# Optimization experiments

Hardware: AMD Instinct MI355X
Metric: run time of the kernel (lower is better)

The kernel has to match this reference:

```python
import jax, jax.numpy as jnp
import numpy as np

B, T, D = 2, 2048, 1024
H = 16
HD = D // H  # head_dim = 64 (kv_rank == embed_dim)
INT4_MIN, INT4_MAX = -8.0, 7.0


def _int4_quant_dequant(x):
    # per-token amax over last dim (head_dim), as in INT4Quantizer with 4-D input
    amax = jnp.max(jnp.abs(x), axis=-1, keepdims=True)
    amax = jnp.maximum(amax, 1e-5)
    scale = amax / 7.0
    q = jnp.clip(jnp.round(x / scale), INT4_MIN, INT4_MAX)  # stored as int8 in cache
    return q * scale


def setup_inputs() -> dict:
    key = jax.random.key(0)
    ks = jax.random.split(key, 11)
    s = 1.0 / np.sqrt(D)
    return {
        "query": jax.random.normal(ks[0], (B, T, D), jnp.float32),
        "key": jax.random.normal(ks[1], (B, T, D), jnp.float32),
        "value": jax.random.normal(ks[2], (B, T, D), jnp.float32),
        "Wq": jax.random.normal(ks[3], (D, D), jnp.float32) * s,
        "bq": jnp.zeros((D,), jnp.float32),
        "Wk": jax.random.normal(ks[4], (D, D), jnp.float32) * s,
        "bk": jnp.zeros((D,), jnp.float32),
        "Wv": jax.random.normal(ks[5], (D, D), jnp.float32) * s,
        "bv": jnp.zeros((D,), jnp.float32),
        "Wo": jax.random.normal(ks[6], (D, D), jnp.float32) * s,
        "bo": jnp.zeros((D,), jnp.float32),
    }


def reference(query, key, value, Wq, bq, Wk, bk, Wv, bv, Wo, bo):
    # projections (nn.Linear: x @ W.T + b)
    q = query @ Wq.T + bq
    k = key @ Wk.T + bk
    v = value @ Wv.T + bv
    # (B, T, D) -> (B, H, T, HD)
    q = q.reshape(B, T, H, HD).transpose(0, 2, 1, 3)
    k = k.reshape(B, T, H, HD).transpose(0, 2, 1, 3)
    v = v.reshape(B, T, H, HD).transpose(0, 2, 1, 3)
    # INT4 quantized KV cache update (use_cache=True): quantize -> scatter into
    # fresh cache -> dequantize the just-written block == quant/dequant of k, v
    k = _int4_quant_dequant(k)
    v = _int4_quant_dequant(v)
    # attention
    scale = HD ** (-0.5)
    attn = jnp.einsum("bhqd,bhkd->bhqk", q, k) * scale
    attn = jax.nn.softmax(attn.astype(jnp.float32), axis=-1).astype(query.dtype)
    out = jnp.einsum("bhqk,bhkd->bhqd", attn, v)
    out = out.transpose(0, 2, 1, 3).reshape(B, T, D)
    out = out @ Wo.T + bo
    return out
```

## Files before the change

### kernel.cpp

```cpp
#include <hip/hip_runtime.h>

typedef unsigned short u16;
typedef unsigned int u32;
typedef float f32x4 __attribute__((ext_vector_type(4)));
typedef float f32x16 __attribute__((ext_vector_type(16)));
typedef short s16x8 __attribute__((ext_vector_type(8)));
typedef u16 u16x8 __attribute__((ext_vector_type(8)));
typedef u16 u16x4 __attribute__((ext_vector_type(4)));
typedef u32 u32x4 __attribute__((ext_vector_type(4)));
typedef _Float16 h16x8 __attribute__((ext_vector_type(8)));
typedef _Float16 h16x2 __attribute__((ext_vector_type(2)));

#define B_ 2
#define T_ 2048
#define H_ 16
#define D_ 1024
#define HD_ 64
#define NTOK (B_*T_)

#define QSCALE 0.18033688011112042f

__device__ __forceinline__ u16 f2b(float f){
  u32 u = __float_as_uint(f);
  return (u16)((u + 0x7fffu + ((u>>16)&1u)) >> 16);
}
__device__ __forceinline__ float b2f(u16 h){ return __uint_as_float(((u32)h)<<16); }

__device__ __forceinline__ void gload_lds16(const u16* g, u16* s){
  __builtin_amdgcn_global_load_lds((const __attribute__((address_space(1))) void*)g,
                                   (__attribute__((address_space(3))) void*)s, 16, 0, 0);
}

template<int ROWS, int WAVES>
__device__ __forceinline__ void stage_tile(const u16* __restrict__ g, size_t ldg,
                                           u16* s, int tid){
  const int w = tid>>6, l = tid&63;
  const int rw = ROWS/WAVES;
  #pragma unroll
  for (int i=0;i<ROWS/(WAVES*8);i++){
    int r0 = w*rw + i*8;
    int r  = r0 + (l>>3);
    int u  = (l&7) ^ (r&7);
    gload_lds16(g + (size_t)r*ldg + (size_t)u*8, s + r0*64);
  }
}

__device__ __forceinline__ u16x8 rfragT(const u16* s, int r, int ks, int hi){
  int phys = (ks*2 + hi) ^ (r&7);
  return *(const u16x8*)(s + r*64 + phys*8);
}

__device__ __forceinline__ void stage_tile32(const u16* __restrict__ g, size_t ldg,
                                             u16* s, int tid){
  const int w = tid>>6, l = tid&63;
  int r0 = w*16;
  int r  = r0 + (l>>2);
  int v  = (l&3) ^ ((r>>1)&3);
  gload_lds16(g + (size_t)r*ldg + (size_t)v*8, s + r0*32);
}
__device__ __forceinline__ u16x8 read_frag32(const u16* s, int r, int l){
  int phys = (l>>4) ^ ((r>>1)&3);
  return *(const u16x8*)(s + r*32 + phys*8);
}

__device__ __forceinline__ f32x4 mfma16_bf16(u16x8 a, u16x8 b, f32x4 c){
  return __builtin_amdgcn_mfma_f32_16x16x32_bf16(
      __builtin_bit_cast(s16x8,a), __builtin_bit_cast(s16x8,b), c, 0,0,0);
}
__device__ __forceinline__ f32x16 mfma32_f16(u16x8 a, u16x8 b, f32x16 c){
  return __builtin_amdgcn_mfma_f32_32x32x16_f16(
      __builtin_bit_cast(h16x8,a), __builtin_bit_cast(h16x8,b), c, 0,0,0);
}

__device__ __forceinline__ float ex2(float x){
#if __has_builtin(__builtin_amdgcn_exp2f)
  return __builtin_amdgcn_exp2f(x);
#else
  return exp2f(x);
#endif
}
__device__ __forceinline__ u32 pk2(float a, float b){
  u16 x = __builtin_bit_cast(u16, (_Float16)a);
  u16 y = __builtin_bit_cast(u16, (_Float16)b);
  return (u32)x | ((u32)y<<16);
}
__device__ __forceinline__ u32 pkrtz(float a, float b){
#if __has_builtin(__builtin_amdgcn_cvt_pkrtz)
  auto r = __builtin_amdgcn_cvt_pkrtz(a, b);
  return __builtin_bit_cast(u32, r);
#else
  return pk2(a, b);
#endif
}

__device__ __forceinline__ void split_bf4(const float* in, u16* hi, u16* lo, int i){
  f32x4 v = ((const f32x4*)in)[i];
  u16x4 h, lw;
  #pragma unroll
  for (int j=0;j<4;j++){
    u16 hb = f2b(v[j]);
    h[j] = hb;
    lw[j] = f2b(v[j] - b2f(hb));
  }
  ((u16x4*)hi)[i] = h;
  ((u16x4*)lo)[i] = lw;
}
__device__ __forceinline__ void split_h4(const float* in, u16* out, int i){
  f32x4 v = ((const f32x4*)in)[i];
  u16x4 o;
  #pragma unroll
  for (int j=0;j<4;j++){
    _Float16 t = (_Float16)v[j];
    o[j] = __builtin_bit_cast(u16, t);
  }
  ((u16x4*)out)[i] = o;
}

__global__ void split_all_kernel(const float* __restrict__ q, const float* __restrict__ k,
                                 const float* __restrict__ v,
                                 const float* __restrict__ wq, const float* __restrict__ wk,
                                 const float* __restrict__ wv, const float* __restrict__ wo,
                                 u16* __restrict__ qh, u16* __restrict__ khi, u16* __restrict__ klo,
                                 u16* __restrict__ vhi, u16* __restrict__ vlo,
                                 u16* __restrict__ wqh, u16* __restrict__ wkh, u16* __restrict__ wkl,
                                 u16* __restrict__ wvh, u16* __restrict__ wvl, u16* __restrict__ woh){
  int i = blockIdx.x*256 + threadIdx.x;
  int which = blockIdx.y;
  if (which < 3){
    if (which==0)      split_h4 (q, qh, i);
    else if (which==1) split_bf4(k, khi, klo, i);
    else               split_bf4(v, vhi, vlo, i);
  } else {
    if (i >= D_*D_/4) return;
    if (which==3)      split_h4 (wq, wqh, i);
    else if (which==4) split_bf4(wk, wkh, wkl, i);
    else if (which==5) split_bf4(wv, wvh, wvl, i);
    else               split_h4 (wo, woh, i);
  }
}

template<int F16OUT>
__global__ __launch_bounds__(256)
void gemm1(const u16* __restrict__ Ah, const u16* __restrict__ Wh,
           const float* __restrict__ bias, void* __restrict__ Cout, float oscale)
{
  __shared__ u16 sA[2][128*64];
  __shared__ u16 sW[2][128*64];
  const int tid = threadIdx.x, l = tid&63, c = l&31, hi = l>>5, w = tid>>6;
  const int wm = w>>1, wn = w&1;
  const int bm = blockIdx.x, bn = blockIdx.y;
  const u16* A0 = Ah + (size_t)bm*128*D_;
  const u16* W0 = Wh + (size_t)bn*128*D_;
  f32x16 acc[2][2] = {};

  stage_tile<128,4>(A0, D_, sA[0], tid);
  stage_tile<128,4>(W0, D_, sW[0], tid);
  __syncthreads();
  for (int t=0; t<D_/64; ++t){
    const int cur = t&1;
    if (t+1 < D_/64){
      stage_tile<128,4>(A0 + (t+1)*64, D_, sA[cur^1], tid);
      stage_tile<128,4>(W0 + (t+1)*64, D_, sW[cur^1], tid);
    }
    #pragma unroll
    for (int kc=0;kc<4;kc++){
      u16x8 af[2], wf[2];
      af[0] = rfragT(sA[cur], wm*64 +      c, kc, hi);
      af[1] = rfragT(sA[cur], wm*64 + 32 + c, kc, hi);
      wf[0] = rfragT(sW[cur], wn*64 +      c, kc, hi);
      wf[1] = rfragT(sW[cur], wn*64 + 32 + c, kc, hi);
      #pragma unroll
      for (int mb=0;mb<2;mb++)
        #pragma unroll
        for (int nb=0;nb<2;nb++)
          acc[mb][nb] = mfma32_f16(af[mb], wf[nb], acc[mb][nb]);
    }
    __syncthreads();
  }

  #pragma unroll
  for (int nb=0;nb<2;nb++){
    int col = bn*128 + wn*64 + nb*32 + c;
    float bv = bias[col];
    #pragma unroll
    for (int mb=0;mb<2;mb++){
      #pragma unroll
      for (int r=0;r<16;r++){
        int row = bm*128 + wm*64 + mb*32 + (r&3) + 8*(r>>2) + 4*hi;
        float v = (acc[mb][nb][r] + bv) * oscale;
        if constexpr (F16OUT){
          ((_Float16*)Cout)[(size_t)row*D_ + col] = (_Float16)v;
        } else {
          ((float*)Cout)[(size_t)row*D_ + col] = v;
        }
      }
    }
  }
}

__global__ __launch_bounds__(512)
void gemm3_quant_kv(const u16* __restrict__ kAh, const u16* __restrict__ kAl,
                    const u16* __restrict__ kWh, const u16* __restrict__ kWl,
                    const float* __restrict__ kbias, u16* __restrict__ kOut,
                    const u16* __restrict__ vAh, const u16* __restrict__ vAl,
                    const u16* __restrict__ vWh, const u16* __restrict__ vWl,
                    const float* __restrict__ vbias, u16* __restrict__ vOut)
{
  extern __shared__ u16 sm[];
  const int tid = threadIdx.x, l = tid&63, w = tid>>6, l15 = l&15, g = l>>4;
  const int wm = w>>1, wn = w&1;
  const int bm = blockIdx.x, bn = blockIdx.y;
  const bool isV = blockIdx.z != 0;
  const u16* Ah = isV ? vAh : kAh;
  const u16* Al = isV ? vAl : kAl;
  const u16* Wh = isV ? vWh : kWh;
  const u16* Wl = isV ? vWl : kWl;
  const float* bias = isV ? vbias : kbias;
  u16* Out = isV ? vOut : kOut;

  const u16* A0 = Ah + (size_t)bm*128*D_;
  const u16* A1 = Al + (size_t)bm*128*D_;
  const u16* W0 = Wh + (size_t)bn*128*D_;
  const u16* W1 = Wl + (size_t)bn*128*D_;
  constexpr int TS = 128*32;
  f32x4 acc[2][4] = {};

  auto stage = [&](int buf, int t){
    u16* base = sm + buf*4*TS;
    stage_tile32(A0 + t*32, D_, base       , tid);
    stage_tile32(A1 + t*32, D_, base +   TS, tid);
    stage_tile32(W0 + t*32, D_, base + 2*TS, tid);
    stage_tile32(W1 + t*32, D_, base + 3*TS, tid);
  };
  stage(0,0);
  __syncthreads();
  for (int t=0; t<D_/32; ++t){
    const int cur = t&1;
    if (t+1 < D_/32) stage(cur^1, t+1);
    const u16* base = sm + cur*4*TS;
    u16x8 ahh[2], ahl[2], whh[4], whl[4];
    #pragma unroll
    for (int fm=0;fm<2;fm++){
      ahh[fm] = read_frag32(base     , wm*32+fm*16+l15, l);
      ahl[fm] = read_frag32(base+  TS, wm*32+fm*16+l15, l);
    }
    #pragma unroll
    for (int fn=0;fn<4;fn++){
      whh[fn] = read_frag32(base+2*TS, wn*64+fn*16+l15, l);
      whl[fn] = read_frag32(base+3*TS, wn*64+fn*16+l15, l);
    }
    #pragma unroll
    for (int fm=0;fm<2;fm++)
      #pragma unroll
      for (int fn=0;fn<4;fn++){
        acc[fm][fn] = mfma16_bf16(ahh[fm], whh[fn], acc[fm][fn]);
        acc[fm][fn] = mfma16_bf16(ahh[fm], whl[fn], acc[fm][fn]);
        acc[fm][fn] = mfma16_bf16(ahl[fm], whh[fn], acc[fm][fn]);
      }
    __syncthreads();
  }

  #pragma unroll
  for (int fn=0;fn<4;fn++){
    float bv = bias[bn*128 + wn*64 + fn*16 + l15];
    #pragma unroll
    for (int fm=0;fm<2;fm++)
      #pragma unroll
      for (int j=0;j<4;j++) acc[fm][fn][j] += bv;
  }

  u16 (*sdq)[136] = (u16(*)[136])sm;
  #pragma unroll
  for (int fm=0;fm<2;fm++)
    #pragma unroll
    for (int j=0;j<4;j++){
      float a = 0.f;
      #pragma unroll
      for (int fn=0;fn<4;fn++) a = fmaxf(a, fabsf(acc[fm][fn][j]));
      a = fmaxf(a, __shfl_xor(a,1)); a = fmaxf(a, __shfl_xor(a,2));
      a = fmaxf(a, __shfl_xor(a,4)); a = fmaxf(a, __shfl_xor(a,8));
      a = fmaxf(a, 1e-5f);
      float scale = a / 7.0f;
      int g2 = ((g&1)<<1) | (g>>1);
      int rowK = wm*32 + fm*16 + g*4  + j;
      int rowV = wm*32 + fm*16 + g2*4 + j;
      #pragma unroll
      for (int fn=0;fn<4;fn++){
        float q = rintf(acc[fm][fn][j] / scale);
        q = fminf(fmaxf(q, -8.f), 7.f);
        _Float16 dq = (_Float16)(q * scale);
        int col = wn*64 + fn*16 + l15;
        if (!isV) sdq[rowK][col] = __builtin_bit_cast(u16, dq);
        else      sdq[col][rowV] = __builtin_bit_cast(u16, dq);
      }
    }
  __syncthreads();

  if (!isV){
    int r = tid>>2, seg = tid&3;
    u16* dst = Out + (size_t)(bm*128 + r)*D_ + bn*128 + seg*32;
    #pragma unroll
    for (int i=0;i<4;i++)
      *(u16x8*)(dst + i*8) = *(const u16x8*)&sdq[r][seg*32 + i*8];
  } else {
    int cc = tid>>2, seg = tid&3;
    int hh = 2*bn + (cc>>6), dd = cc&63, b = bm>>4;
    u16* dst = Out + ((size_t)((b*H_+hh)*HD_ + dd))*T_ + (bm&15)*128 + seg*32;
    #pragma unroll
    for (int i=0;i<4;i++)
      *(u16x8*)(dst + i*8) = *(const u16x8*)&sdq[cc][seg*32 + i*8];
  }
}

__global__ __launch_bounds__(256, 4)
void attn_kernel(const _Float16* __restrict__ Qp, const u16* __restrict__ Kdq,
                 const u16* __restrict__ Vt, u16* __restrict__ po,
                 float* __restrict__ pl)
{
  __shared__ u16 sK[2][64*64];
  __shared__ u16 sV[2][64*64];
  const int tid = threadIdx.x, l = tid&63, c = l&31, hi = l>>5, w = tid>>6;
  const int dsp = blockIdx.x;
  const int xcd = dsp & 7, slot = dsp >> 3;
  const int bh = xcd*4 + (slot>>5);
  const int rem = slot & 31;
  const int qb = rem >> 1, sp = rem & 1;
  const int b = bh>>4, h = bh&15;

  u16x8 qf[4];
  {
    const u16* qrow = (const u16*)Qp + (size_t)(b*T_ + qb*128 + w*32 + c)*D_ + h*HD_;
    #pragma unroll
    for (int ks=0;ks<4;ks++)
      qf[ks] = *(const u16x8*)(qrow + ks*16 + hi*8);
  }

  f32x16 o0 = {}, o1 = {};
  float lsp = 0.f;

  const u16* Kb = Kdq + (size_t)(b*T_ + sp*1024)*D_ + h*HD_;
  const u16* Vb = Vt  + (size_t)(bh*HD_)*T_ + sp*1024;

  stage_tile<64,4>(Kb, D_, sK[0], tid);
  stage_tile<64,4>(Vb, T_, sV[0], tid);
  __syncthreads();

  for (int kt=0; kt<16; kt++){
    const int cur = kt&1;
    if (kt+1 < 16){
      stage_tile<64,4>(Kb + (size_t)((kt+1)*64)*D_, D_, sK[cur^1], tid);
      stage_tile<64,4>(Vb + (kt+1)*64,              T_, sV[cur^1], tid);
    }
    const u16* sKc = sK[cur];
    const u16* sVc = sV[cur];

    u16x8 vf0[4], vf1[4];
    #pragma unroll
    for (int ch=0; ch<4; ch++){
      vf0[ch] = rfragT(sVc,      c, ch, hi);
      vf1[ch] = rfragT(sVc, 32 + c, ch, hi);
    }

    #pragma unroll
    for (int kb=0;kb<2;kb++){
      f32x16 s = {};
      #pragma unroll
      for (int ks=0;ks<4;ks++){
        u16x8 kf = rfragT(sKc, kb*32 + c, ks, hi);
        s = mfma32_f16(kf, qf[ks], s);
      }
      float p[16];
      #pragma unroll
      for (int r=0;r<16;r++) p[r] = ex2(s[r]);
      {
        float t0 = (p[0]+p[1]) + (p[2]+p[3]);
        float t1 = (p[4]+p[5]) + (p[6]+p[7]);
        float t2 = (p[8]+p[9]) + (p[10]+p[11]);
        float t3 = (p[12]+p[13]) + (p[14]+p[15]);
        lsp += (t0+t1) + (t2+t3);
      }
      u32x4 pw0 = { pkrtz(p[0],p[1]),  pkrtz(p[2],p[3]),
                    pkrtz(p[4],p[5]),  pkrtz(p[6],p[7]) };
      u32x4 pw1 = { pkrtz(p[8],p[9]),  pkrtz(p[10],p[11]),
                    pkrtz(p[12],p[13]),pkrtz(p[14],p[15]) };
      u16x8 pa0 = __builtin_bit_cast(u16x8, pw0);
      u16x8 pa1 = __builtin_bit_cast(u16x8, pw1);
      o0 = mfma32_f16(pa0, vf0[kb*2+0], o0);
      o0 = mfma32_f16(pa1, vf0[kb*2+1], o0);
      o1 = mfma32_f16(pa0, vf1[kb*2+0], o1);
      o1 = mfma32_f16(pa1, vf1[kb*2+1], o1);
    }
    __syncthreads();
  }

  float lt = lsp + __shfl_xor(lsp, 32);
  if (hi == 0) pl[(size_t)(sp*32 + bh)*T_ + qb*128 + w*32 + c] = lt;

  u16* pob = po + ((size_t)(sp*32 + bh)*T_ + qb*128 + w*32)*HD_;
  #pragma unroll
  for (int r=0;r<16;r++){
    int crow = (r&3) + 8*(r>>2) + 4*hi;
    pob[crow*HD_ + c]      = __builtin_bit_cast(u16, (_Float16)o0[r]);
    pob[crow*HD_ + 32 + c] = __builtin_bit_cast(u16, (_Float16)o1[r]);
  }
}

__global__ __launch_bounds__(256)
void combine_kernel(const u16* __restrict__ po, const float* __restrict__ pl,
                    u16* __restrict__ Ao)
{
  const int dsp = blockIdx.x;
  const int xcd = dsp & 7, slot = dsp >> 3;
  const int bh = xcd*4 + (slot>>6);
  const int inner = slot & 63;
  int item = inner*256 + threadIdx.x;
  int d8 = item & 7, t = item >> 3;
  size_t r0 = ((size_t)bh*T_ + t);
  size_t r1 = r0 + (size_t)32*T_;
  h16x8 a = *(const h16x8*)(po + r0*HD_ + d8*8);
  h16x8 bb = *(const h16x8*)(po + r1*HD_ + d8*8);
  float lt = pl[r0] + pl[r1];
  float rl = 1.0f / lt;
  u16x8 o;
  #pragma unroll
  for (int j=0;j<8;j++)
    o[j] = __builtin_bit_cast(u16, (_Float16)(((float)a[j] + (float)bb[j])*rl));
  int b = bh>>4, h = bh&15;
  *(u16x8*)(Ao + ((size_t)(b*T_ + t))*D_ + h*HD_ + d8*8) = o;
}

extern "C" void kernel_launch(void* const* d_in, const int* in_sizes, int n_in,
                              void* d_out, int out_size, void* d_ws, size_t ws_size,
                              hipStream_t stream)
{
  (void)in_sizes; (void)n_in; (void)out_size; (void)ws_size;
  const float* query = (const float*)d_in[0];
  const float* key   = (const float*)d_in[1];
  const float* value = (const float*)d_in[2];
  const float* Wq = (const float*)d_in[3];
  const float* bq = (const float*)d_in[4];
  const float* Wk = (const float*)d_in[5];
  const float* bk = (const float*)d_in[6];
  const float* Wv = (const float*)d_in[7];
  const float* bv = (const float*)d_in[8];
  const float* Wo = (const float*)d_in[9];
  const float* bo = (const float*)d_in[10];
  float* out = (float*)d_out;

  char* p = (char*)d_ws;
  auto take = [&](size_t n){ char* r = p; p += (n + 255) & ~(size_t)255; return r; };
  const size_t big = (size_t)NTOK*D_*2;
  const size_t wsz = (size_t)D_*D_*2;

  u16* q_h  = (u16*)take(big);
  u16* khi  = (u16*)take(big);  u16* klo = (u16*)take(big);
  u16* vhi  = (u16*)take(big);  u16* vlo = (u16*)take(big);
  u16* wq_h = (u16*)take(wsz);
  u16* wkh  = (u16*)take(wsz);  u16* wkl = (u16*)take(wsz);
  u16* wvh  = (u16*)take(wsz);  u16* wvl = (u16*)take(wsz);
  u16* wo_h = (u16*)take(wsz);
  u16*  Qp  = (u16*)take(big);
  u16*  Kdq = (u16*)take(big);
  u16*  Vtp = (u16*)take(big);
  u16*  Ao  = (u16*)take(big);

  u16*   po = khi;
  float* pl = (float*)wq_h;

  split_all_kernel<<<dim3(NTOK*D_/4/256, 7), 256, 0, stream>>>(
      query, key, value, Wq, Wk, Wv, Wo,
      q_h, khi, klo, vhi, vlo,
      wq_h, wkh, wkl, wvh, wvl, wo_h);

  gemm1<1><<<dim3(32,8), 256, 0, stream>>>(q_h, wq_h, bq, Qp, QSCALE);

  gemm3_quant_kv<<<dim3(32,8,2), 512, 64*1024, stream>>>(
      khi, klo, wkh, wkl, bk, Kdq,
      vhi, vlo, wvh, wvl, bv, Vtp);

  attn_kernel<<<1024, 256, 0, stream>>>((const _Float16*)Qp, Kdq, Vtp, po, pl);
  combine_kernel<<<2048, 256, 0, stream>>>(po, pl, Ao);

  gemm1<0><<<dim3(32,8), 256, 0, stream>>>(Ao, wo_h, bo, out, 1.0f);
}
```

Baseline: 174.4 us.

## Fuse K/V fp32 to bf16 hi/lo split into the KV projection GEMM

The K and V activations are no longer pre-split into bf16 hi/lo buffers by the split kernel. The KV GEMM now stages the raw fp32 tiles into shared memory and does the hi/lo decomposition in registers while reading fragments. This removes a full read and two writes of the K/V activation tensors plus their re-read, at the cost of extra ALU work in the GEMM inner loop. The hi part is now formed by truncation rather than rounding, and the shared-memory layout changes to a swizzled fp32 A tile. The attention partial buffers get their own workspace because they can no longer alias the removed split buffers.

After: 173.9 us. About the same (-0.3%).

```diff
diff --git a/kernel.cpp b/kernel.cpp
--- a/kernel.cpp
+++ b/kernel.cpp
@@ -116,27 +116,20 @@
   ((u16x4*)out)[i] = o;
 }
 
-__global__ void split_all_kernel(const float* __restrict__ q, const float* __restrict__ k,
-                                 const float* __restrict__ v,
+__global__ void split_all_kernel(const float* __restrict__ q,
                                  const float* __restrict__ wq, const float* __restrict__ wk,
                                  const float* __restrict__ wv, const float* __restrict__ wo,
-                                 u16* __restrict__ qh, u16* __restrict__ khi, u16* __restrict__ klo,
-                                 u16* __restrict__ vhi, u16* __restrict__ vlo,
+                                 u16* __restrict__ qh,
                                  u16* __restrict__ wqh, u16* __restrict__ wkh, u16* __restrict__ wkl,
                                  u16* __restrict__ wvh, u16* __restrict__ wvl, u16* __restrict__ woh){
   int i = blockIdx.x*256 + threadIdx.x;
   int which = blockIdx.y;
-  if (which < 3){
-    if (which==0)      split_h4 (q, qh, i);
-    else if (which==1) split_bf4(k, khi, klo, i);
-    else               split_bf4(v, vhi, vlo, i);
-  } else {
-    if (i >= D_*D_/4) return;
-    if (which==3)      split_h4 (wq, wqh, i);
-    else if (which==4) split_bf4(wk, wkh, wkl, i);
-    else if (which==5) split_bf4(wv, wvh, wvl, i);
-    else               split_h4 (wo, woh, i);
-  }
+  if (which==0){ split_h4(q, qh, i); return; }
+  if (i >= D_*D_/4) return;
+  if (which==1)      split_h4 (wq, wqh, i);
+  else if (which==2) split_bf4(wk, wkh, wkl, i);
+  else if (which==3) split_bf4(wv, wvh, wvl, i);
+  else               split_h4 (wo, woh, i);
 }
 
 template<int F16OUT>
@@ -199,55 +192,67 @@
 }
 
 __global__ __launch_bounds__(512)
-void gemm3_quant_kv(const u16* __restrict__ kAh, const u16* __restrict__ kAl,
-                    const u16* __restrict__ kWh, const u16* __restrict__ kWl,
-                    const float* __restrict__ kbias, u16* __restrict__ kOut,
-                    const u16* __restrict__ vAh, const u16* __restrict__ vAl,
-                    const u16* __restrict__ vWh, const u16* __restrict__ vWl,
-                    const float* __restrict__ vbias, u16* __restrict__ vOut)
+void gemm3_quant_kv(const float* __restrict__ kA, const u16* __restrict__ kWh,
+                    const u16* __restrict__ kWl, const float* __restrict__ kbias,
+                    u16* __restrict__ kOut,
+                    const float* __restrict__ vA, const u16* __restrict__ vWh,
+                    const u16* __restrict__ vWl, const float* __restrict__ vbias,
+                    u16* __restrict__ vOut)
 {
   extern __shared__ u16 sm[];
   const int tid = threadIdx.x, l = tid&63, w = tid>>6, l15 = l&15, g = l>>4;
   const int wm = w>>1, wn = w&1;
   const int bm = blockIdx.x, bn = blockIdx.y;
   const bool isV = blockIdx.z != 0;
-  const u16* Ah = isV ? vAh : kAh;
-  const u16* Al = isV ? vAl : kAl;
+  const float* Af = isV ? vA : kA;
   const u16* Wh = isV ? vWh : kWh;
   const u16* Wl = isV ? vWl : kWl;
   const float* bias = isV ? vbias : kbias;
   u16* Out = isV ? vOut : kOut;
 
-  const u16* A0 = Ah + (size_t)bm*128*D_;
-  const u16* A1 = Al + (size_t)bm*128*D_;
+  const u16* A0u = (const u16*)(Af + (size_t)bm*128*D_);
   const u16* W0 = Wh + (size_t)bn*128*D_;
   const u16* W1 = Wl + (size_t)bn*128*D_;
-  constexpr int TS = 128*32;
+  constexpr int BUF = 16384;
   f32x4 acc[2][4] = {};
 
   auto stage = [&](int buf, int t){
-    u16* base = sm + buf*4*TS;
-    stage_tile32(A0 + t*32, D_, base       , tid);
-    stage_tile32(A1 + t*32, D_, base +   TS, tid);
-    stage_tile32(W0 + t*32, D_, base + 2*TS, tid);
-    stage_tile32(W1 + t*32, D_, base + 3*TS, tid);
+    u16* base = sm + buf*BUF;
+    stage_tile<128,8>(A0u + t*64, 2048, base, tid);
+    stage_tile32(W0 + t*32, D_, base +  8192, tid);
+    stage_tile32(W1 + t*32, D_, base + 12288, tid);
   };
   stage(0,0);
   __syncthreads();
   for (int t=0; t<D_/32; ++t){
     const int cur = t&1;
     if (t+1 < D_/32) stage(cur^1, t+1);
-    const u16* base = sm + cur*4*TS;
-    u16x8 ahh[2], ahl[2], whh[4], whl[4];
+    const u16* base = sm + cur*BUF;
+    u16x8 ahh[2], ahl[2];
     #pragma unroll
     for (int fm=0;fm<2;fm++){
-      ahh[fm] = read_frag32(base     , wm*32+fm*16+l15, l);
-      ahl[fm] = read_frag32(base+  TS, wm*32+fm*16+l15, l);
-    }
+      int r = wm*32 + fm*16 + l15;
+      int rx = r&7;
+      const u16* row = base + r*64;
+      f32x4 x0 = *(const f32x4*)(row + (((g*2  )^rx)*8));
+      f32x4 x1 = *(const f32x4*)(row + (((g*2+1)^rx)*8));
+      u16x8 hh, ll;
+      #pragma unroll
+      for (int j=0;j<4;j++){
+        u32 b0 = __float_as_uint(x0[j]);
+        hh[j]   = (u16)(b0>>16);
+        ll[j]   = f2b(x0[j] - __uint_as_float(b0 & 0xffff0000u));
+        u32 b1 = __float_as_uint(x1[j]);
+        hh[j+4] = (u16)(b1>>16);
+        ll[j+4] = f2b(x1[j] - __uint_as_float(b1 & 0xffff0000u));
+      }
+      ahh[fm] = hh; ahl[fm] = ll;
+    }
+    u16x8 whh[4], whl[4];
     #pragma unroll
     for (int fn=0;fn<4;fn++){
-      whh[fn] = read_frag32(base+2*TS, wn*64+fn*16+l15, l);
-      whl[fn] = read_frag32(base+3*TS, wn*64+fn*16+l15, l);
+      whh[fn] = read_frag32(base +  8192, wn*64+fn*16+l15, l);
+      whl[fn] = read_frag32(base + 12288, wn*64+fn*16+l15, l);
     }
     #pragma unroll
     for (int fm=0;fm<2;fm++)
@@ -453,8 +458,6 @@
   const size_t wsz = (size_t)D_*D_*2;
 
   u16* q_h  = (u16*)take(big);
-  u16* khi  = (u16*)take(big);  u16* klo = (u16*)take(big);
-  u16* vhi  = (u16*)take(big);  u16* vlo = (u16*)take(big);
   u16* wq_h = (u16*)take(wsz);
   u16* wkh  = (u16*)take(wsz);  u16* wkl = (u16*)take(wsz);
   u16* wvh  = (u16*)take(wsz);  u16* wvl = (u16*)take(wsz);
@@ -463,20 +466,18 @@
   u16*  Kdq = (u16*)take(big);
   u16*  Vtp = (u16*)take(big);
   u16*  Ao  = (u16*)take(big);
-
-  u16*   po = khi;
-  float* pl = (float*)wq_h;
-
-  split_all_kernel<<<dim3(NTOK*D_/4/256, 7), 256, 0, stream>>>(
-      query, key, value, Wq, Wk, Wv, Wo,
-      q_h, khi, klo, vhi, vlo,
-      wq_h, wkh, wkl, wvh, wvl, wo_h);
+  u16*  po  = (u16*)take(big*2);
+  float* pl = (float*)take((size_t)64*T_*4);
+
+  split_all_kernel<<<dim3(NTOK*D_/4/256, 5), 256, 0, stream>>>(
+      query, Wq, Wk, Wv, Wo,
+      q_h, wq_h, wkh, wkl, wvh, wvl, wo_h);
 
   gemm1<1><<<dim3(32,8), 256, 0, stream>>>(q_h, wq_h, bq, Qp, QSCALE);
 
   gemm3_quant_kv<<<dim3(32,8,2), 512, 64*1024, stream>>>(
-      khi, klo, wkh, wkl, bk, Kdq,
-      vhi, vlo, wvh, wvl, bv, Vtp);
+      key,   wkh, wkl, bk, Kdq,
+      value, wvh, wvl, bv, Vtp);
 
   attn_kernel<<<1024, 256, 0, stream>>>((const _Float16*)Qp, Kdq, Vtp, po, pl);
   combine_kernel<<<2048, 256, 0, stream>>>(po, pl, Ao);
```
